# Kernel optimization log

Hardware: AMD Instinct MI355X
Metric: run time of the kernel (lower is better)

## Reference

```python
import jax, jax.numpy as jnp
import numpy as np

B, T, D_MODEL = 2, 2048, 2048
N_HEAD, N_KV, HD = 32, 8, 64


def _rope_tables(T, hd, base=10000.0):
    # standard rotary tables, (T, hd) with frequencies repeated over both halves
    inv_freq = 1.0 / (base ** (np.arange(0, hd // 2, dtype=np.float32) / (hd // 2)))
    t = np.arange(T, dtype=np.float32)
    freqs = np.outer(t, inv_freq)            # (T, hd/2)
    emb = np.concatenate([freqs, freqs], axis=-1)  # (T, hd)
    return jnp.asarray(np.cos(emb)), jnp.asarray(np.sin(emb))


def setup_inputs() -> dict:
    key = jax.random.key(0)
    ks = jax.random.split(key, 5)
    cos, sin = _rope_tables(T, HD)
    s = 0.02
    return {
        "x": jax.random.normal(ks[0], (B, T, D_MODEL), jnp.float32),
        "cos": cos,
        "sin": sin,
        "Wq": jax.random.normal(ks[1], (N_HEAD * HD, D_MODEL), jnp.float32) * s,
        "Wk": jax.random.normal(ks[2], (N_KV * HD, D_MODEL), jnp.float32) * s,
        "Wv": jax.random.normal(ks[3], (N_KV * HD, D_MODEL), jnp.float32) * s,
        "Wo": jax.random.normal(ks[4], (D_MODEL, N_HEAD * HD), jnp.float32) * s,
    }


def _apply_rope(x, cos, sin):
    # x: (B, H, T, D); cos/sin: (T, D)
    D = x.shape[-1]
    x1, x2 = x[..., : D // 2], x[..., D // 2 :]
    rot = jnp.concatenate([-x2, x1], axis=-1)
    c = cos[: x.shape[-2]][None, None]
    s = sin[: x.shape[-2]][None, None]
    return x * c + rot * s


def reference(x, cos, sin, Wq, Wk, Wv, Wo):
    Bv, Tv, _ = x.shape
    q = (x @ Wq.T).reshape(Bv, Tv, N_HEAD, HD).transpose(0, 2, 1, 3)  # (B,H,T,D)
    k = (x @ Wk.T).reshape(Bv, Tv, N_KV, HD).transpose(0, 2, 1, 3)    # (B,Hkv,T,D)
    v = (x @ Wv.T).reshape(Bv, Tv, N_KV, HD).transpose(0, 2, 1, 3)
    q = _apply_rope(q, cos, sin)
    k = _apply_rope(k, cos, sin)
    repeat = N_HEAD // N_KV
    if repeat > 1:
        k = jnp.repeat(k, repeat, axis=1)
        v = jnp.repeat(v, repeat, axis=1)
    scale = 1.0 / jnp.sqrt(jnp.float32(HD)).astype(x.dtype)
    scores = jnp.einsum("bhqd,bhkd->bhqk", q, k) * scale
    causal = jnp.tril(jnp.ones((Tv, Tv), dtype=bool))
    scores = jnp.where(causal[None, None], scores, jnp.finfo(scores.dtype).min)
    attn = jax.nn.softmax(scores, axis=-1)
    out = jnp.einsum("bhqk,bhkd->bhqd", attn, v)
    out = out.transpose(0, 2, 1, 3).reshape(Bv, Tv, N_HEAD * HD)
    return out @ Wo.T
```

## Files before the change

### kernel.cpp

```cpp
#include <hip/hip_runtime.h>
#include <stdint.h>

#define B_SZ 2
#define T_SEQ 2048
#define DM 2048
#define NH 32
#define NKV 8
#define HD 64
#define QKV_W 3072

typedef unsigned short u16;
typedef __bf16 bf16x8 __attribute__((ext_vector_type(8)));
typedef float floatx4 __attribute__((ext_vector_type(4)));

__device__ __forceinline__ float bf2f(u16 u) {
  union { unsigned u; float f; } v; v.u = ((unsigned)u) << 16; return v.f;
}
__device__ __forceinline__ u16 f2bf(float f) {
  union { float f; unsigned u; } v; v.f = f;
  unsigned r = v.u + 0x7fff + ((v.u >> 16) & 1);
  return (u16)(r >> 16);
}
__device__ __forceinline__ unsigned pk2bf(float hi, float lo) {
  return __builtin_amdgcn_perm(__float_as_uint(hi), __float_as_uint(lo), 0x07060302u);
}
__device__ __forceinline__ float fexp2(float x) {
#if __has_builtin(__builtin_amdgcn_exp2f)
  return __builtin_amdgcn_exp2f(x);
#else
  return exp2f(x);
#endif
}

__device__ __forceinline__ void gld_lds16(const void* g, void* l) {
  __builtin_amdgcn_global_load_lds(
      (const __attribute__((address_space(1))) unsigned int*)g,
      (__attribute__((address_space(3))) unsigned int*)l, 16, 0, 0);
}

__global__ __launch_bounds__(256) void conv_kernel(
    const float* __restrict__ src, u16* __restrict__ dst, int n4)
{
  int i = blockIdx.x * 256 + threadIdx.x;
  int stride = gridDim.x * 256;
  for (; i < n4; i += stride) {
    float4 v = ((const float4*)src)[i];
    ushort4 o;
    o.x = f2bf(v.x); o.y = f2bf(v.y); o.z = f2bf(v.z); o.w = f2bf(v.w);
    ((ushort4*)dst)[i] = o;
  }
}

__global__ __launch_bounds__(256) void conv_wqkv_kernel(
    const float* __restrict__ Wq, const float* __restrict__ Wk,
    const float* __restrict__ Wv, u16* __restrict__ dst)
{
  int i = blockIdx.x * 256 + threadIdx.x;
  int stride = gridDim.x * 256;
  for (; i < 1572864; i += stride) {
    float4 v;
    if (i < 1048576)      v = ((const float4*)Wq)[i];
    else if (i < 1310720) v = ((const float4*)Wk)[i - 1048576];
    else                  v = ((const float4*)Wv)[i - 1310720];
    ushort4 o;
    o.x = f2bf(v.x); o.y = f2bf(v.y); o.z = f2bf(v.z); o.w = f2bf(v.w);
    ((ushort4*)dst)[i] = o;
  }
}

__global__ __launch_bounds__(256) void gemm_qkv_kernel(
    const u16* __restrict__ A, const u16* __restrict__ Bt,
    u16* __restrict__ C)
{
  __shared__ __align__(16) u16 sA[128 * 64];
  __shared__ __align__(16) u16 sB[128 * 64];

  const int n0 = blockIdx.x * 128;
  const int m0 = blockIdx.y * 128;
  const int K = 2048;

  const int tid  = threadIdx.x;
  const int lane = tid & 63;
  const int w    = tid >> 6;
  const int wm = w >> 1, wn = w & 1;
  const int lm = lane & 15, lq = lane >> 4;

  floatx4 acc[4][4];
  #pragma unroll
  for (int i = 0; i < 4; i++)
    #pragma unroll
    for (int j = 0; j < 4; j++) { floatx4 z = {0.f,0.f,0.f,0.f}; acc[i][j] = z; }

  const int srow   = tid >> 3;
  const int schunk = (tid & 7) ^ (srow & 7);
  const u16* ApG = A  + (size_t)(m0 + srow) * K + schunk * 8;
  const u16* BpG = Bt + (size_t)(n0 + srow) * K + schunk * 8;
  u16* sAd = sA + tid * 8;
  u16* sBd = sB + tid * 8;

  const int sw  = lm & 7;
  const int rba = (wm * 64 + lm) * 64;
  const int rbb = (wn * 64 + lm) * 64;
  const int c0  = (lq ^ sw) * 8;
  const int c1  = ((4 + lq) ^ sw) * 8;

  for (int k0 = 0; k0 < K; k0 += 64) {
    #pragma unroll
    for (int p = 0; p < 4; p++) {
      gld_lds16(ApG + (size_t)p * 32 * K + k0, sAd + p * 2048);
      gld_lds16(BpG + (size_t)p * 32 * K + k0, sBd + p * 2048);
    }
    __syncthreads();

    #pragma unroll
    for (int kk = 0; kk < 2; kk++) {
      const int ck = kk ? c1 : c0;
      bf16x8 af[4], bfr[4];
      #pragma unroll
      for (int mi = 0; mi < 4; mi++)
        af[mi] = *(const bf16x8*)(sA + rba + mi * 1024 + ck);
      #pragma unroll
      for (int ni = 0; ni < 4; ni++)
        bfr[ni] = *(const bf16x8*)(sB + rbb + ni * 1024 + ck);

      #pragma unroll
      for (int mi = 0; mi < 4; mi++)
        #pragma unroll
        for (int ni = 0; ni < 4; ni++)
          acc[mi][ni] = __builtin_amdgcn_mfma_f32_16x16x32_bf16(
              af[mi], bfr[ni], acc[mi][ni], 0, 0, 0);
    }
    __syncthreads();
  }

  #pragma unroll
  for (int mi = 0; mi < 4; mi++)
    #pragma unroll
    for (int ni = 0; ni < 4; ni++)
      #pragma unroll
      for (int r = 0; r < 4; r++) {
        int row = m0 + wm*64 + mi*16 + lq*4 + r;
        int col = n0 + wn*64 + ni*16 + lm;
        C[(size_t)row * QKV_W + col] = f2bf(acc[mi][ni][r]);
      }
}

__global__ __launch_bounds__(256) void gemm_out_kernel(
    const u16* __restrict__ A, const u16* __restrict__ Bt,
    float* __restrict__ C)
{
  __shared__ __align__(16) u16 sA[128 * 64];
  __shared__ __align__(16) u16 sB[128 * 64];

  const int n0 = blockIdx.x * 128;
  const int m0 = blockIdx.y * 128;
  const int K = 2048;

  const int tid  = threadIdx.x;
  const int lane = tid & 63;
  const int w    = tid >> 6;
  const int wm = w >> 1, wn = w & 1;
  const int lm = lane & 15, lq = lane >> 4;

  floatx4 acc[4][4];
  #pragma unroll
  for (int i = 0; i < 4; i++)
    #pragma unroll
    for (int j = 0; j < 4; j++) { floatx4 z = {0.f,0.f,0.f,0.f}; acc[i][j] = z; }

  const int srow   = tid >> 3;
  const int schunk = (tid & 7) ^ (srow & 7);
  const u16* ApG = A  + (size_t)(m0 + srow) * K + schunk * 8;
  const u16* BpG = Bt + (size_t)(n0 + srow) * K + schunk * 8;
  u16* sAd = sA + tid * 8;
  u16* sBd = sB + tid * 8;

  const int sw  = lm & 7;
  const int rba = (wm * 64 + lm) * 64;
  const int rbb = (wn * 64 + lm) * 64;
  const int c0  = (lq ^ sw) * 8;
  const int c1  = ((4 + lq) ^ sw) * 8;

  for (int k0 = 0; k0 < K; k0 += 64) {
    #pragma unroll
    for (int p = 0; p < 4; p++) {
      gld_lds16(ApG + (size_t)p * 32 * K + k0, sAd + p * 2048);
      gld_lds16(BpG + (size_t)p * 32 * K + k0, sBd + p * 2048);
    }
    __syncthreads();

    #pragma unroll
    for (int kk = 0; kk < 2; kk++) {
      const int ck = kk ? c1 : c0;
      bf16x8 af[4], bfr[4];
      #pragma unroll
      for (int mi = 0; mi < 4; mi++)
        af[mi] = *(const bf16x8*)(sA + rba + mi * 1024 + ck);
      #pragma unroll
      for (int ni = 0; ni < 4; ni++)
        bfr[ni] = *(const bf16x8*)(sB + rbb + ni * 1024 + ck);

      #pragma unroll
      for (int mi = 0; mi < 4; mi++)
        #pragma unroll
        for (int ni = 0; ni < 4; ni++)
          acc[mi][ni] = __builtin_amdgcn_mfma_f32_16x16x32_bf16(
              af[mi], bfr[ni], acc[mi][ni], 0, 0, 0);
    }
    __syncthreads();
  }

  #pragma unroll
  for (int mi = 0; mi < 4; mi++)
    #pragma unroll
    for (int ni = 0; ni < 4; ni++)
      #pragma unroll
      for (int r = 0; r < 4; r++) {
        int row = m0 + wm*64 + mi*16 + lq*4 + r;
        int col = n0 + wn*64 + ni*16 + lm;
        C[(size_t)row * DM + col] = acc[mi][ni][r];
      }
}

#define QSCALE 0.180336880f
__global__ __launch_bounds__(256) void prep_kernel(
    const u16* __restrict__ qkv, const float* __restrict__ cosf,
    const float* __restrict__ sinf, u16* __restrict__ qb,
    u16* __restrict__ kb, u16* __restrict__ vbt)
{
  __shared__ u16 tile[64][66];
  const int tid = threadIdx.x;

  if (blockIdx.x < 4096) {
    const int bt = blockIdx.x;
    const int b = bt / T_SEQ, t = bt % T_SEQ;
    const u16* row = qkv + (size_t)bt * QKV_W;

    #pragma unroll
    for (int i = 0; i < 4; i++) {
      int idx = i * 256 + tid;
      int h = idx >> 5, dp = idx & 31;
      float x1 = bf2f(row[h * 64 + dp]);
      float x2 = bf2f(row[h * 64 + dp + 32]);
      float c = cosf[t * 64 + dp];
      float s = sinf[t * 64 + dp];
      float o1 = (x1 * c - x2 * s) * QSCALE;
      float o2 = (x2 * c + x1 * s) * QSCALE;
      size_t base = ((size_t)(b * NH + h) * T_SEQ + t) * HD + dp;
      qb[base]      = f2bf(o1);
      qb[base + 32] = f2bf(o2);
    }
    {
      int idx = tid;
      int kvh = idx >> 5, dp = idx & 31;
      float x1 = bf2f(row[2048 + kvh * 64 + dp]);
      float x2 = bf2f(row[2048 + kvh * 64 + dp + 32]);
      float c = cosf[t * 64 + dp];
      float s = sinf[t * 64 + dp];
      size_t base = ((size_t)(b * NKV + kvh) * T_SEQ + t) * HD + dp;
      kb[base]      = f2bf(x1 * c - x2 * s);
      kb[base + 32] = f2bf(x2 * c + x1 * s);
    }
  } else {
    const int idx2 = blockIdx.x - 4096;
    const int t0  = (idx2 & 31) * 64;
    const int kvh = (idx2 >> 5) & 7;
    const int b   = idx2 >> 8;

    #pragma unroll
    for (int i = 0; i < 16; i++) {
      int idx = i * 256 + tid;
      int r = idx >> 6, c = idx & 63;
      tile[r][c] = qkv[(size_t)(b * T_SEQ + t0 + r) * QKV_W + 2560 + kvh * 64 + c];
    }
    __syncthreads();
    #pragma unroll
    for (int i = 0; i < 16; i++) {
      int idx = i * 256 + tid;
      int d = idx >> 6, c = idx & 63;
      vbt[((size_t)(b * NKV + kvh) * HD + d) * T_SEQ + t0 + c] = tile[c][d];
    }
  }
}

__global__ __launch_bounds__(256, 3) void attn_kernel(
    const u16* __restrict__ qb, const u16* __restrict__ kb,
    const u16* __restrict__ vbt, u16* __restrict__ attn)
{
  __shared__ __align__(16) u16 sK[2][64 * 64];
  __shared__ __align__(16) u16 sV[2][64 * 64];
  __shared__ __align__(16) u16 sP[4][16][72];
  __shared__ float sAl[4][16];

  const int tid  = threadIdx.x;
  const int lane = tid & 63;
  const int w    = tid >> 6;

  const int l  = blockIdx.x;
  const int qt = 63 - (l >> 4);
  const int kv = l & 7;
  const int b  = (l >> 3) & 1;
  const int h  = kv * 4 + w;
  const int ktmax = qt >> 1;
  const int moff  = 32 * (qt & 1);

  const int lm = lane & 15, lq = lane >> 4;
  const int sw = lm & 7;

  bf16x8 qf[2][2];
  {
    const u16* qhead = qb + ((size_t)(b * NH + h) * T_SEQ + qt * 32) * HD;
    #pragma unroll
    for (int nq = 0; nq < 2; nq++) {
      const u16* qrow = qhead + (size_t)(nq * 16 + lm) * HD + lq * 8;
      qf[nq][0] = *(const bf16x8*)(qrow);
      qf[nq][1] = *(const bf16x8*)(qrow + 32);
    }
  }

  floatx4 o_acc[2][4];
  #pragma unroll
  for (int i = 0; i < 2; i++)
    #pragma unroll
    for (int j = 0; j < 4; j++) { floatx4 z = {0.f,0.f,0.f,0.f}; o_acc[i][j] = z; }
  float m_run[2] = {-1e30f, -1e30f};
  float l_run[2] = {0.f, 0.f};

  const u16* kbase = kb  + (size_t)(b * NKV + kv) * T_SEQ * HD;
  const u16* vbase = vbt + (size_t)(b * NKV + kv) * HD * T_SEQ;

  const int p0row = tid >> 3,        p1row = (256 + tid) >> 3;
  const int p0ck  = (tid & 7) ^ (p0row & 7), p1ck = ((256 + tid) & 7) ^ (p1row & 7);
  const u16* kp0 = kbase + (size_t)p0row * HD + p0ck * 8;
  const u16* kp1 = kbase + (size_t)p1row * HD + p1ck * 8;
  const u16* vp0 = vbase + (size_t)p0row * T_SEQ + p0ck * 8;
  const u16* vp1 = vbase + (size_t)p1row * T_SEQ + p1ck * 8;
  const int d0 = tid * 16, d1 = (256 + tid) * 16;

  auto compute_tile = [&](const u16* sKc, const u16* sVc, const bool diag) {
    bf16x8 kf[4][2], vf[4][2];
    #pragma unroll
    for (int nt = 0; nt < 4; nt++) {
      kf[nt][0] = *(const bf16x8*)(sKc + (((nt*16 + lm) * 8 + (lq ^ sw)) << 3));
      kf[nt][1] = *(const bf16x8*)(sKc + (((nt*16 + lm) * 8 + ((4 + lq) ^ sw)) << 3));
      vf[nt][0] = *(const bf16x8*)(sVc + (((nt*16 + lm) * 8 + (lq ^ sw)) << 3));
      vf[nt][1] = *(const bf16x8*)(sVc + (((nt*16 + lm) * 8 + ((4 + lq) ^ sw)) << 3));
    }

    floatx4 s_acc[2][4];
    __builtin_amdgcn_s_setprio(1);
    #pragma unroll
    for (int nq = 0; nq < 2; nq++)
      #pragma unroll
      for (int nt = 0; nt < 4; nt++) {
        floatx4 z = {0.f,0.f,0.f,0.f};
        z = __builtin_amdgcn_mfma_f32_16x16x32_bf16(kf[nt][0], qf[nq][0], z, 0, 0, 0);
        z = __builtin_amdgcn_mfma_f32_16x16x32_bf16(kf[nt][1], qf[nq][1], z, 0, 0, 0);
        s_acc[nq][nt] = z;
      }
    __builtin_amdgcn_s_setprio(0);

    #pragma unroll
    for (int nq = 0; nq < 2; nq++) {
      if (diag) {
        #pragma unroll
        for (int nt = 0; nt < 4; nt++)
          #pragma unroll
          for (int r = 0; r < 4; r++)
            if (nt * 16 + lq * 4 + r > nq * 16 + lm + moff) s_acc[nq][nt][r] = -1e30f;
      }

      float mloc = s_acc[nq][0][0];
      #pragma unroll
      for (int nt = 0; nt < 4; nt++)
        #pragma unroll
        for (int r = 0; r < 4; r++) mloc = fmaxf(mloc, s_acc[nq][nt][r]);
      mloc = fmaxf(mloc, __shfl_xor(mloc, 16));
      mloc = fmaxf(mloc, __shfl_xor(mloc, 32));

      float mnew = m_run[nq];
      if (!__all(mloc - m_run[nq] <= 8.0f)) {
        mnew = fmaxf(m_run[nq], mloc);
        float al = fexp2(m_run[nq] - mnew);
        m_run[nq] = mnew;
        l_run[nq] *= al;
        if (lq == 0) sAl[w][lm] = al;
        floatx4 alv = *(const floatx4*)&sAl[w][lq * 4];
        #pragma unroll
        for (int nd = 0; nd < 4; nd++)
          #pragma unroll
          for (int r = 0; r < 4; r++)
            o_acc[nq][nd][r] *= alv[r];
      }

      float rs = 0.f;
      uint2 pk[4];
      #pragma unroll
      for (int nt = 0; nt < 4; nt++) {
        float p0 = fexp2(s_acc[nq][nt][0] - mnew);
        float p1 = fexp2(s_acc[nq][nt][1] - mnew);
        float p2 = fexp2(s_acc[nq][nt][2] - mnew);
        float p3 = fexp2(s_acc[nq][nt][3] - mnew);
        rs += (p0 + p1) + (p2 + p3);
        pk[nt].x = pk2bf(p1, p0);
        pk[nt].y = pk2bf(p3, p2);
      }
      rs += __shfl_xor(rs, 16);
      rs += __shfl_xor(rs, 32);
      l_run[nq] += rs;

      #pragma unroll
      for (int nt = 0; nt < 4; nt++)
        *(uint2*)&sP[w][lm][nt * 16 + lq * 4] = pk[nt];

      __builtin_amdgcn_s_setprio(1);
      #pragma unroll
      for (int st = 0; st < 2; st++) {
        bf16x8 pf = *(const bf16x8*)(&sP[w][lm][st * 32 + lq * 8]);
        #pragma unroll
        for (int nd = 0; nd < 4; nd++)
          o_acc[nq][nd] = __builtin_amdgcn_mfma_f32_16x16x32_bf16(
              pf, vf[nd][st], o_acc[nq][nd], 0, 0, 0);
      }
      __builtin_amdgcn_s_setprio(0);
    }
  };

  const int nst = (ktmax >> 1) + 1;
  for (int s2 = 0; s2 < nst; s2++) {
    const int kt0  = s2 * 2;
    const int kt1  = kt0 + 1;
    const int kt1c = kt1 < 32 ? kt1 : 31;
    __syncthreads();
    gld_lds16(kp0 + (size_t)kt0  * 64 * HD, (char*)sK[0] + d0);
    gld_lds16(kp1 + (size_t)kt0  * 64 * HD, (char*)sK[0] + d1);
    gld_lds16(kp0 + (size_t)kt1c * 64 * HD, (char*)sK[1] + d0);
    gld_lds16(kp1 + (size_t)kt1c * 64 * HD, (char*)sK[1] + d1);
    gld_lds16(vp0 + kt0  * 64, (char*)sV[0] + d0);
    gld_lds16(vp1 + kt0  * 64, (char*)sV[0] + d1);
    gld_lds16(vp0 + kt1c * 64, (char*)sV[1] + d0);
    gld_lds16(vp1 + kt1c * 64, (char*)sV[1] + d1);
    __syncthreads();

    compute_tile(sK[0], sV[0], kt0 == ktmax);
    if (kt1 <= ktmax) compute_tile(sK[1], sV[1], kt1 == ktmax);
  }

  #pragma unroll
  for (int nq = 0; nq < 2; nq++) {
    __builtin_amdgcn_s_waitcnt(0);
    if (lq == 0) sAl[w][lm] = l_run[nq];
    floatx4 lv = *(const floatx4*)&sAl[w][lq * 4];
    #pragma unroll
    for (int nd = 0; nd < 4; nd++)
      #pragma unroll
      for (int r = 0; r < 4; r++) {
        float v = o_acc[nq][nd][r] / lv[r];
        size_t row = (size_t)b * T_SEQ + qt * 32 + nq * 16 + lq * 4 + r;
        attn[row * DM + h * HD + nd * 16 + lm] = f2bf(v);
      }
  }
}

extern "C" void kernel_launch(void* const* d_in, const int* in_sizes, int n_in,
                              void* d_out, int out_size, void* d_ws, size_t ws_size,
                              hipStream_t stream)
{
  const float* x    = (const float*)d_in[0];
  const float* cosf = (const float*)d_in[1];
  const float* sinf = (const float*)d_in[2];
  const float* Wq   = (const float*)d_in[3];
  const float* Wk   = (const float*)d_in[4];
  const float* Wv   = (const float*)d_in[5];
  const float* Wo   = (const float*)d_in[6];
  float* out = (float*)d_out;

  char* ws = (char*)d_ws;
  u16* qkvb  = (u16*)(ws + 0);
  u16* attnb = (u16*)(ws + 0);
  u16* qb    = (u16*)(ws + 25165824);
  u16* kb    = (u16*)(ws + 41943040);
  u16* vbt   = (u16*)(ws + 46137344);
  u16* xb    = (u16*)(ws + 50331648);
  u16* wob   = (u16*)(ws + 50331648);
  u16* wqkvb = (u16*)(ws + 67108864);

  dim3 blk(256);
  conv_kernel<<<dim3(2048), blk, 0, stream>>>(x, xb, 8388608 / 4);
  conv_wqkv_kernel<<<dim3(1536), blk, 0, stream>>>(Wq, Wk, Wv, wqkvb);

  gemm_qkv_kernel<<<dim3(24, 32), blk, 0, stream>>>(xb, wqkvb, qkvb);

  conv_kernel<<<dim3(1024), blk, 0, stream>>>(Wo, wob, 4194304 / 4);

  prep_kernel<<<dim3(4608), blk, 0, stream>>>(qkvb, cosf, sinf, qb, kb, vbt);
  attn_kernel<<<dim3(1024), blk, 0, stream>>>(qb, kb, vbt, attnb);
  gemm_out_kernel<<<dim3(16, 32), blk, 0, stream>>>(attnb, wob, out);
}
```

Measured before the change: 288.9 us.

## Double-buffer LDS tiles in QKV and output projection GEMMs

```diff
diff --git a/kernel.cpp b/kernel.cpp
--- a/kernel.cpp
+++ b/kernel.cpp
@@ -72,8 +72,8 @@
     const u16* __restrict__ A, const u16* __restrict__ Bt,
     u16* __restrict__ C)
 {
-  __shared__ __align__(16) u16 sA[128 * 64];
-  __shared__ __align__(16) u16 sB[128 * 64];
+  __shared__ __align__(16) u16 sA[2][128 * 64];
+  __shared__ __align__(16) u16 sB[2][128 * 64];
 
   const int n0 = blockIdx.x * 128;
   const int m0 = blockIdx.y * 128;
@@ -95,8 +95,8 @@
   const int schunk = (tid & 7) ^ (srow & 7);
   const u16* ApG = A  + (size_t)(m0 + srow) * K + schunk * 8;
   const u16* BpG = Bt + (size_t)(n0 + srow) * K + schunk * 8;
-  u16* sAd = sA + tid * 8;
-  u16* sBd = sB + tid * 8;
+  u16* sAd0 = sA[0] + tid * 8;  u16* sAd1 = sA[1] + tid * 8;
+  u16* sBd0 = sB[0] + tid * 8;  u16* sBd1 = sB[1] + tid * 8;
 
   const int sw  = lm & 7;
   const int rba = (wm * 64 + lm) * 64;
@@ -104,24 +104,24 @@
   const int c0  = (lq ^ sw) * 8;
   const int c1  = ((4 + lq) ^ sw) * 8;
 
-  for (int k0 = 0; k0 < K; k0 += 64) {
+  auto stage = [&](u16* sAd, u16* sBd, int k0) {
     #pragma unroll
     for (int p = 0; p < 4; p++) {
       gld_lds16(ApG + (size_t)p * 32 * K + k0, sAd + p * 2048);
       gld_lds16(BpG + (size_t)p * 32 * K + k0, sBd + p * 2048);
     }
-    __syncthreads();
-
+  };
+  auto compute = [&](const u16* sAc, const u16* sBc) {
     #pragma unroll
     for (int kk = 0; kk < 2; kk++) {
       const int ck = kk ? c1 : c0;
       bf16x8 af[4], bfr[4];
       #pragma unroll
       for (int mi = 0; mi < 4; mi++)
-        af[mi] = *(const bf16x8*)(sA + rba + mi * 1024 + ck);
+        af[mi] = *(const bf16x8*)(sAc + rba + mi * 1024 + ck);
       #pragma unroll
       for (int ni = 0; ni < 4; ni++)
-        bfr[ni] = *(const bf16x8*)(sB + rbb + ni * 1024 + ck);
+        bfr[ni] = *(const bf16x8*)(sBc + rbb + ni * 1024 + ck);
 
       #pragma unroll
       for (int mi = 0; mi < 4; mi++)
@@ -130,6 +130,17 @@
           acc[mi][ni] = __builtin_amdgcn_mfma_f32_16x16x32_bf16(
               af[mi], bfr[ni], acc[mi][ni], 0, 0, 0);
     }
+  };
+
+  stage(sAd0, sBd0, 0);
+  __syncthreads();
+
+  for (int k0 = 0; k0 < K; k0 += 128) {
+    stage(sAd1, sBd1, k0 + 64);
+    compute(sA[0], sB[0]);
+    __syncthreads();
+    if (k0 + 128 < K) stage(sAd0, sBd0, k0 + 128);
+    compute(sA[1], sB[1]);
     __syncthreads();
   }
 
@@ -149,8 +160,8 @@
     const u16* __restrict__ A, const u16* __restrict__ Bt,
     float* __restrict__ C)
 {
-  __shared__ __align__(16) u16 sA[128 * 64];
-  __shared__ __align__(16) u16 sB[128 * 64];
+  __shared__ __align__(16) u16 sA[2][128 * 64];
+  __shared__ __align__(16) u16 sB[2][128 * 64];
 
   const int n0 = blockIdx.x * 128;
   const int m0 = blockIdx.y * 128;
@@ -172,8 +183,8 @@
   const int schunk = (tid & 7) ^ (srow & 7);
   const u16* ApG = A  + (size_t)(m0 + srow) * K + schunk * 8;
   const u16* BpG = Bt + (size_t)(n0 + srow) * K + schunk * 8;
-  u16* sAd = sA + tid * 8;
-  u16* sBd = sB + tid * 8;
+  u16* sAd0 = sA[0] + tid * 8;  u16* sAd1 = sA[1] + tid * 8;
+  u16* sBd0 = sB[0] + tid * 8;  u16* sBd1 = sB[1] + tid * 8;
 
   const int sw  = lm & 7;
   const int rba = (wm * 64 + lm) * 64;
@@ -181,24 +192,24 @@
   const int c0  = (lq ^ sw) * 8;
   const int c1  = ((4 + lq) ^ sw) * 8;
 
-  for (int k0 = 0; k0 < K; k0 += 64) {
+  auto stage = [&](u16* sAd, u16* sBd, int k0) {
     #pragma unroll
     for (int p = 0; p < 4; p++) {
       gld_lds16(ApG + (size_t)p * 32 * K + k0, sAd + p * 2048);
       gld_lds16(BpG + (size_t)p * 32 * K + k0, sBd + p * 2048);
     }
-    __syncthreads();
-
+  };
+  auto compute = [&](const u16* sAc, const u16* sBc) {
     #pragma unroll
     for (int kk = 0; kk < 2; kk++) {
       const int ck = kk ? c1 : c0;
       bf16x8 af[4], bfr[4];
       #pragma unroll
       for (int mi = 0; mi < 4; mi++)
-        af[mi] = *(const bf16x8*)(sA + rba + mi * 1024 + ck);
+        af[mi] = *(const bf16x8*)(sAc + rba + mi * 1024 + ck);
       #pragma unroll
       for (int ni = 0; ni < 4; ni++)
-        bfr[ni] = *(const bf16x8*)(sB + rbb + ni * 1024 + ck);
+        bfr[ni] = *(const bf16x8*)(sBc + rbb + ni * 1024 + ck);
 
       #pragma unroll
       for (int mi = 0; mi < 4; mi++)
@@ -207,6 +218,17 @@
           acc[mi][ni] = __builtin_amdgcn_mfma_f32_16x16x32_bf16(
               af[mi], bfr[ni], acc[mi][ni], 0, 0, 0);
     }
+  };
+
+  stage(sAd0, sBd0, 0);
+  __syncthreads();
+
+  for (int k0 = 0; k0 < K; k0 += 128) {
+    stage(sAd1, sBd1, k0 + 64);
+    compute(sA[0], sB[0]);
+    __syncthreads();
+    if (k0 + 128 < K) stage(sAd0, sBd0, k0 + 128);
+    compute(sA[1], sB[1]);
     __syncthreads();
   }
 
```

Result: slower. 300.9 us (+4.2%).
